# Kernel optimization log

Hardware: AMD Instinct MI355X
Metric: run time of the kernel (lower is better)

Reference implementation:

```python
import jax, jax.numpy as jnp
import numpy as np

B, S, IN_D, OUT_D, QD = 4, 1024, 16, 16, 32
HID, HEADS, HD, L, TED = 256, 8, 32, 4, 256
DECAY = 0.1
SCALE = HD ** -0.5


def _ln(x):
    m = x.mean(-1, keepdims=True)
    v = ((x - m) ** 2).mean(-1, keepdims=True)
    return (x - m) * jax.lax.rsqrt(v + 1e-5)


def _lin(x, w, b):
    # torch nn.Linear: y = x @ W^T + b, W is [out, in]
    return jnp.einsum('...i,oi->...o', x, w) + b


def _sin_emb(t, dim):
    half = dim // 2
    freqs = jnp.exp(-np.log(10000.0) * jnp.arange(half, dtype=jnp.float32) / (half - 1))
    a = t[:, None] * freqs[None, :]
    return jnp.concatenate([jnp.sin(a), jnp.cos(a)], axis=-1)


def _mish(x):
    return x * jnp.tanh(jax.nn.softplus(x))


def _gelu(x):
    return jax.nn.gelu(x, approximate=False)


def setup_inputs() -> dict:
    key = jax.random.key(0)
    ks = iter(jax.random.split(key, 64))

    def w(shape):
        return jax.random.normal(next(ks), shape, dtype=jnp.float32) * 0.02

    d = {}
    d['x'] = jax.random.normal(next(ks), (B, S, IN_D), dtype=jnp.float32)
    d['query'] = jax.random.normal(next(ks), (B, QD), dtype=jnp.float32)
    d['time'] = jax.random.uniform(next(ks), (B,), dtype=jnp.float32) * 1000.0
    d['tm_w1'] = w((TED * 4, TED)); d['tm_b1'] = jnp.zeros((TED * 4,), jnp.float32)
    d['tm_w2'] = w((TED, TED * 4)); d['tm_b2'] = jnp.zeros((TED,), jnp.float32)
    d['in_w'] = w((HID, IN_D)); d['in_b'] = jnp.zeros((HID,), jnp.float32)
    d['q_w1'] = w((HID, QD)); d['q_b1'] = jnp.zeros((HID,), jnp.float32)
    d['q_w2'] = w((HID, HID)); d['q_b2'] = jnp.zeros((HID,), jnp.float32)
    d['n1_w'] = jnp.ones((L, HID), jnp.float32); d['n1_b'] = jnp.zeros((L, HID), jnp.float32)
    d['qkv_w'] = w((L, 3 * HID, HID)); d['qkv_b'] = jnp.zeros((L, 3 * HID), jnp.float32)
    d['ap_w'] = w((L, HID, HID)); d['ap_b'] = jnp.zeros((L, HID), jnp.float32)
    d['rel_bias'] = w((L, 2 * S - 1, HEADS))
    d['n2_w'] = jnp.ones((L, HID), jnp.float32); d['n2_b'] = jnp.zeros((L, HID), jnp.float32)
    d['f1_w'] = w((L, 4 * HID, HID)); d['f1_b'] = jnp.zeros((L, 4 * HID), jnp.float32)
    d['f2_w'] = w((L, HID, 4 * HID)); d['f2_b'] = jnp.zeros((L, HID), jnp.float32)
    d['t1_w'] = w((L, HID, TED)); d['t1_b'] = jnp.zeros((L, HID), jnp.float32)
    d['t2_w'] = w((L, HID, HID)); d['t2_b'] = jnp.zeros((L, HID), jnp.float32)
    d['out_w'] = w((OUT_D, HID)); d['out_b'] = jnp.zeros((OUT_D,), jnp.float32)
    return d


def reference(x, query, time, tm_w1, tm_b1, tm_w2, tm_b2, in_w, in_b,
              q_w1, q_b1, q_w2, q_b2, n1_w, n1_b, qkv_w, qkv_b, ap_w, ap_b,
              rel_bias, n2_w, n2_b, f1_w, f1_b, f2_w, f2_b, t1_w, t1_b,
              t2_w, t2_b, out_w, out_b):
    Bx, Sx, _ = x.shape
    # time MLP: SinusoidalPosEmb -> Linear -> Mish -> Linear
    te = _lin(_sin_emb(time, TED), tm_w1, tm_b1)
    te = _lin(_mish(te), tm_w2, tm_b2)            # [B, TED]
    # input projection + query conditioning (relative-pos path: no abs pos emb)
    h = _lin(x, in_w, in_b)                        # [B, S, HID]
    qe = _lin(_gelu(_lin(query, q_w1, q_b1)), q_w2, q_b2)
    h = h + qe[:, None, :]
    # shared relative-distance structures
    idx = jnp.arange(Sx)
    rel = idx[:, None] - idx[None, :]              # [S, S]
    dec = jnp.exp(-DECAY * jnp.abs(rel).astype(jnp.float32))
    rel_idx = rel + S - 1                          # index into 2*max_seq_len-1 table
    for l in range(L):
        # time conditioning per block
        tp = _lin(_gelu(_lin(te, t1_w[l], t1_b[l])), t2_w[l], t2_b[l])
        xn = _ln(h + tp[:, None, :]) * n1_w[l] + n1_b[l]
        qkv = _lin(xn, qkv_w[l], qkv_b[l]).reshape(Bx, Sx, 3, HEADS, HD)
        qkv = qkv.transpose(2, 0, 3, 1, 4)          # [3, B, H, S, hd]
        q_, k_, v_ = qkv[0], qkv[1], qkv[2]
        attn = jnp.einsum('bhqd,bhkd->bhqk', q_, k_) * SCALE
        bias = rel_bias[l][rel_idx]                 # [S, S, H]
        attn = attn + (dec[:, :, None] * bias).transpose(2, 0, 1)[None]
        a = jax.nn.softmax(attn, axis=-1)
        o = jnp.einsum('bhqk,bhkd->bhqd', a, v_)
        o = o.transpose(0, 2, 1, 3).reshape(Bx, Sx, HID)
        h = h + _lin(o, ap_w[l], ap_b[l])           # residual from pre-time x
        xn2 = _ln(h) * n2_w[l] + n2_b[l]
        h = h + _lin(_gelu(_lin(xn2, f1_w[l], f1_b[l])), f2_w[l], f2_b[l])
    return _lin(h, out_w, out_b)
```

## Files before the change

kernel.cpp:

```cpp
#include <hip/hip_runtime.h>
#include <hip/hip_bf16.h>
#include <math.h>

#define S_LEN 1024
#define HID 256
#define HEADS 8
#define HD 32
#define NLAYER 4
#define TED 256
#define BATCH 4
#define DECAY 0.1f
#define ATT_SCALE 0.17677669529663687f
#define LOG2E 1.4426950408889634f

typedef __bf16 bf8_t __attribute__((ext_vector_type(8)));
typedef float f4_t __attribute__((ext_vector_type(4)));

__device__ __forceinline__ float gelu_f(float x) {
  return 0.5f * x * (1.f + erff(x * 0.70710678118654752f));
}
__device__ __forceinline__ __bf16 f2bf(float f) { return (__bf16)f; }

__global__ __launch_bounds__(256) void k_prep_a(
    const float* __restrict__ timev,
    const float* __restrict__ tm_w1, const float* __restrict__ tm_b1,
    const float* __restrict__ query,
    const float* __restrict__ q_w1, const float* __restrict__ q_b1,
    float* __restrict__ te1, float* __restrict__ q1) {
  int bid = blockIdx.x;
  int lane = threadIdx.x & 63;
  if (bid < 1024) {
    int r = bid * 4 + (threadIdx.x >> 6);
    int o = r & 1023, b = r >> 10;
    float t = timev[b];
    float ev[4];
#pragma unroll
    for (int e = 0; e < 4; e++) {
      int k = lane * 4 + e;
      int i = k & 127;
      float f = __expf(-logf(10000.f) * (float)i / 127.f);
      float a = t * f;
      ev[e] = (k < 128) ? sinf(a) : cosf(a);
    }
    const float* w = tm_w1 + (size_t)o * 256 + lane * 4;
    float4 w4 = *(const float4*)w;
    float s = ev[0] * w4.x + ev[1] * w4.y + ev[2] * w4.z + ev[3] * w4.w;
#pragma unroll
    for (int off = 32; off; off >>= 1) s += __shfl_xor(s, off);
    if (lane == 0) {
      s += tm_b1[o];
      float sp = (s > 20.f) ? s : log1pf(__expf(s));
      te1[r] = s * tanhf(sp);
    }
  } else {
    int r = (bid - 1024) * 4 + (threadIdx.x >> 6);
    int o = r & 255, b = r >> 8;
    float s = 0.f;
    if (lane < 8) {
      float4 a4 = *(const float4*)(query + b * 32 + lane * 4);
      float4 w4 = *(const float4*)(q_w1 + (size_t)o * 32 + lane * 4);
      s = a4.x * w4.x + a4.y * w4.y + a4.z * w4.z + a4.w * w4.w;
    }
#pragma unroll
    for (int off = 32; off; off >>= 1) s += __shfl_xor(s, off);
    if (lane == 0) q1[r] = gelu_f(s + q_b1[o]);
  }
}

__global__ __launch_bounds__(256) void k_prep_b(
    const float* __restrict__ te1, const float* __restrict__ tm_w2,
    const float* __restrict__ tm_b2,
    const float* __restrict__ q1, const float* __restrict__ q_w2,
    const float* __restrict__ q_b2,
    float* __restrict__ te, float* __restrict__ qe) {
  int bid = blockIdx.x;
  int lane = threadIdx.x & 63;
  bool iste = bid < 256;
  int r = (iste ? bid : bid - 256) * 4 + (threadIdx.x >> 6);
  int o = r & 255, b = r >> 8;
  int K = iste ? 1024 : 256;
  const float* a = (iste ? te1 : q1) + (size_t)b * K;
  const float* w = (iste ? tm_w2 : q_w2) + (size_t)o * K;
  float s = 0.f;
  for (int k = lane * 4; k < K; k += 256) {
    float4 a4 = *(const float4*)(a + k);
    float4 w4 = *(const float4*)(w + k);
    s += a4.x * w4.x + a4.y * w4.y + a4.z * w4.z + a4.w * w4.w;
  }
#pragma unroll
  for (int off = 32; off; off >>= 1) s += __shfl_xor(s, off);
  if (lane == 0) {
    s += (iste ? tm_b2 : q_b2)[o];
    (iste ? te : qe)[r] = s;
  }
}

template <int ACT, bool APG>
__global__ __launch_bounds__(256) void k_gemv(
    const float* __restrict__ A, const float* __restrict__ W,
    const float* __restrict__ bias, float* __restrict__ out,
    int K, int OUT) {
  int r = blockIdx.x * 4 + (threadIdx.x >> 6);
  int lane = threadIdx.x & 63;
  int o = r % OUT;
  int b = (r / OUT) % BATCH;
  int g = r / (OUT * BATCH);
  const float* a = A + (size_t)((APG ? g * BATCH : 0) + b) * K;
  const float* w = W + (size_t)(g * OUT + o) * K;
  float s = 0.f;
  for (int k = lane * 4; k < K; k += 256) {
    float4 a4 = *(const float4*)(a + k);
    float4 w4 = *(const float4*)(w + k);
    s += a4.x * w4.x + a4.y * w4.y + a4.z * w4.z + a4.w * w4.w;
  }
#pragma unroll
  for (int off = 32; off; off >>= 1) s += __shfl_xor(s, off);
  if (lane == 0) {
    s += bias[g * OUT + o];
    if (ACT == 1) s = gelu_f(s);
    if (ACT == 2) {
      float sp = (s > 20.f) ? s : log1pf(__expf(s));
      s = s * tanhf(sp);
    }
    out[r] = s;
  }
}

__global__ __launch_bounds__(256) void k_inproj(
    const float* __restrict__ x, const float* __restrict__ in_w,
    const float* __restrict__ in_b, const float* __restrict__ qe,
    float* __restrict__ h) {
  int row = blockIdx.x;
  int b = row >> 10;
  int j = threadIdx.x;
  __shared__ float xr[16];
  if (j < 16) xr[j] = x[row * 16 + j];
  __syncthreads();
  float s = in_b[j] + qe[b * 256 + j];
  const float* w = in_w + j * 16;
#pragma unroll
  for (int i = 0; i < 16; i++) s += xr[i] * w[i];
  h[(size_t)row * 256 + j] = s;
}

__global__ __launch_bounds__(256) void k_cvtall(
    const float* __restrict__ s0, __bf16* __restrict__ d0,
    const float* __restrict__ s1, __bf16* __restrict__ d1,
    const float* __restrict__ s2, __bf16* __restrict__ d2,
    const float* __restrict__ s3, __bf16* __restrict__ d3,
    const float* __restrict__ relb, float* __restrict__ decb_t) {
  int bid = blockIdx.x;
  if (bid >= 1536) {
    int lb = bid - 1536;
    int l = lb >> 6;
    int i = (lb & 63) * 256 + threadIdx.x;
    if (i < 2047 * 8) {
      int idx = i >> 3, hh = i & 7;
      float dec = __expf(-DECAY * fabsf((float)(idx - 1023)));
      decb_t[(l * 8 + hh) * 2048 + idx] = dec * relb[(size_t)l * 2047 * 8 + i] * LOG2E;
    }
    return;
  }
  const float* s; __bf16* d; int base;
  if (bid < 384)       { s = s0; d = d0; base = bid; }
  else if (bid < 512)  { s = s1; d = d1; base = bid - 384; }
  else if (bid < 1024) { s = s2; d = d2; base = bid - 512; }
  else                 { s = s3; d = d3; base = bid - 1024; }
  int i = (base * 256 + threadIdx.x) * 8;
  float4 a = *(const float4*)(s + i);
  float4 b = *(const float4*)(s + i + 4);
  bf8_t o;
  o[0] = f2bf(a.x); o[1] = f2bf(a.y); o[2] = f2bf(a.z); o[3] = f2bf(a.w);
  o[4] = f2bf(b.x); o[5] = f2bf(b.y); o[6] = f2bf(b.z); o[7] = f2bf(b.w);
  *(bf8_t*)(d + i) = o;
}

template <int BN, int ACT, int OUTMODE, bool HASTP>
__global__ __launch_bounds__(256) void k_gemm_lnf(
    const float* __restrict__ h, const __bf16* __restrict__ W,
    const float* __restrict__ bias, void* __restrict__ Cv,
    const float* __restrict__ tp, const float* __restrict__ lw,
    const float* __restrict__ lb, int N) {
  constexpr int K = 256;
  constexpr int NJ = (BN / 2) / 16;
  constexpr int BQ = BN / 64;
  __shared__ __bf16 Al[64 * 264];
  __shared__ __bf16 Bl[2 * BN * 32];
  int tid = threadIdx.x;
  int w = tid >> 6, lane = tid & 63;
  int g = lane >> 4, c = lane & 15;
  int n0 = blockIdx.x * BN, m0 = blockIdx.y * 64;

  int srow = tid >> 2;
  int scol = (tid & 3) * 8;
  int sw = (((tid & 3) ^ ((tid >> 3) & 3))) * 8;
  const __bf16* Wb = W + (size_t)n0 * K + scol;
  bf8_t nB[2][BQ];
#pragma unroll
  for (int sub = 0; sub < 2; sub++)
#pragma unroll
    for (int q = 0; q < BQ; q++)
      nB[sub][q] = *(const bf8_t*)(Wb + (size_t)(q * 64 + srow) * K + sub * 32);

  int sub32 = tid & 31, lrow = tid >> 5;
  int colb = sub32 * 8;
  float4 lw0 = *(const float4*)(lw + colb), lw1 = *(const float4*)(lw + colb + 4);
  float4 lb0 = *(const float4*)(lb + colb), lb1 = *(const float4*)(lb + colb + 4);
  float4 tp0, tp1;
  if (HASTP) {
    const float* tpr = tp + (m0 >> 10) * 256 + colb;
    tp0 = *(const float4*)tpr; tp1 = *(const float4*)(tpr + 4);
  }
#pragma unroll
  for (int p = 0; p < 8; p++) {
    int row = p * 8 + lrow;
    const float* hr = h + (size_t)(m0 + row) * 256 + colb;
    float4 a = *(const float4*)hr;
    float4 b2 = *(const float4*)(hr + 4);
    if (HASTP) {
      a.x += tp0.x; a.y += tp0.y; a.z += tp0.z; a.w += tp0.w;
      b2.x += tp1.x; b2.y += tp1.y; b2.z += tp1.z; b2.w += tp1.w;
    }
    float sum = a.x + a.y + a.z + a.w + b2.x + b2.y + b2.z + b2.w;
    float ss = a.x * a.x + a.y * a.y + a.z * a.z + a.w * a.w +
               b2.x * b2.x + b2.y * b2.y + b2.z * b2.z + b2.w * b2.w;
#pragma unroll
    for (int m = 1; m < 32; m <<= 1) {
      sum += __shfl_xor(sum, m);
      ss += __shfl_xor(ss, m);
    }
    float mean = sum * (1.f / 256.f);
    float var = ss * (1.f / 256.f) - mean * mean;
    float rs = rsqrtf(var + 1e-5f);
    bf8_t o;
    o[0] = f2bf((a.x - mean) * rs * lw0.x + lb0.x);
    o[1] = f2bf((a.y - mean) * rs * lw0.y + lb0.y);
    o[2] = f2bf((a.z - mean) * rs * lw0.z + lb0.z);
    o[3] = f2bf((a.w - mean) * rs * lw0.w + lb0.w);
    o[4] = f2bf((b2.x - mean) * rs * lw1.x + lb1.x);
    o[5] = f2bf((b2.y - mean) * rs * lw1.y + lb1.y);
    o[6] = f2bf((b2.z - mean) * rs * lw1.z + lb1.z);
    o[7] = f2bf((b2.w - mean) * rs * lw1.w + lb1.w);
    *(bf8_t*)&Al[row * 264 + colb] = o;
  }

  int wr = (w >> 1) * 32, wc = (w & 1) * (BN / 2);
  int aseg = ((g ^ ((c >> 1) & 3))) * 8;
  f4_t acc[2][NJ];
#pragma unroll
  for (int i = 0; i < 2; i++)
#pragma unroll
    for (int j = 0; j < NJ; j++) acc[i][j] = (f4_t){0.f, 0.f, 0.f, 0.f};

#pragma unroll
  for (int ph = 0; ph < 4; ph++) {
    __syncthreads();
#pragma unroll
    for (int sub = 0; sub < 2; sub++)
#pragma unroll
      for (int q = 0; q < BQ; q++)
        *(bf8_t*)&Bl[sub * BN * 32 + (q * 64 + srow) * 32 + sw] = nB[sub][q];
    __syncthreads();
    if (ph < 3) {
#pragma unroll
      for (int sub = 0; sub < 2; sub++)
#pragma unroll
        for (int q = 0; q < BQ; q++)
          nB[sub][q] = *(const bf8_t*)(Wb + (size_t)(q * 64 + srow) * K +
                                       (ph + 1) * 64 + sub * 32);
    }
#pragma unroll
    for (int sub = 0; sub < 2; sub++) {
      bf8_t af[2], bfr[NJ];
#pragma unroll
      for (int i = 0; i < 2; i++)
        af[i] = *(const bf8_t*)&Al[(wr + i * 16 + c) * 264 + ph * 64 + sub * 32 + g * 8];
#pragma unroll
      for (int j = 0; j < NJ; j++)
        bfr[j] = *(const bf8_t*)&Bl[sub * BN * 32 + (wc + j * 16 + c) * 32 + aseg];
#pragma unroll
      for (int i = 0; i < 2; i++)
#pragma unroll
        for (int j = 0; j < NJ; j++)
          acc[i][j] = __builtin_amdgcn_mfma_f32_16x16x32_bf16(af[i], bfr[j], acc[i][j], 0, 0, 0);
    }
  }
#pragma unroll
  for (int j = 0; j < NJ; j++) {
    int col = n0 + wc + j * 16 + c;
    float bv = bias[col];
#pragma unroll
    for (int i = 0; i < 2; i++) {
#pragma unroll
      for (int rr = 0; rr < 4; rr++) {
        int row = m0 + wr + i * 16 + 4 * g + rr;
        float v = acc[i][j][rr] + bv;
        if (ACT == 1) v = gelu_f(v);
        size_t idx = (size_t)row * N + col;
        if (OUTMODE == 1) ((float*)Cv)[idx] += v;
        else ((__bf16*)Cv)[idx] = f2bf(v);
      }
    }
  }
}

template <int BM, int BN, int ACT, int OUTMODE, int SPLITK, int KSTEPS>
__global__ __launch_bounds__(256) void k_gemm_mfma(
    const __bf16* __restrict__ A, const __bf16* __restrict__ W,
    const float* __restrict__ bias, void* __restrict__ Cv,
    int M, int N, int K) {
  constexpr int MI = (BM / 2) / 16, NJ = (BN / 2) / 16;
  constexpr int AQ = BM / 64, BQ = BN / 64;
  __shared__ __bf16 Al[BM * 32];
  __shared__ __bf16 Bl[BN * 32];
  int tid = threadIdx.x;
  int w = tid >> 6, lane = tid & 63;
  int g = lane >> 4, c = lane & 15;
  int n0 = blockIdx.x * BN, m0 = blockIdx.y * BM;
  int kbeg = blockIdx.z * KSTEPS * 32;
  int wr = (w >> 1) * (BM / 2), wc = (w & 1) * (BN / 2);
  int srow = tid >> 2;
  int scol = (tid & 3) * 8;
  int sw = (((tid & 3) ^ ((tid >> 3) & 3))) * 8;
  int aseg = ((g ^ ((c >> 1) & 3))) * 8;

  f4_t acc[MI][NJ];
#pragma unroll
  for (int i = 0; i < MI; i++)
#pragma unroll
    for (int j = 0; j < NJ; j++) acc[i][j] = (f4_t){0.f, 0.f, 0.f, 0.f};

  const __bf16* Ab = A + (size_t)m0 * K + scol + kbeg;
  const __bf16* Wb = W + (size_t)n0 * K + scol + kbeg;

  bf8_t nA[AQ], nB[BQ];
#pragma unroll
  for (int q = 0; q < AQ; q++)
    nA[q] = *(const bf8_t*)(Ab + (size_t)(q * 64 + srow) * K);
#pragma unroll
  for (int q = 0; q < BQ; q++)
    nB[q] = *(const bf8_t*)(Wb + (size_t)(q * 64 + srow) * K);

#pragma unroll
  for (int ks = 0; ks < KSTEPS; ks++) {
    __syncthreads();
#pragma unroll
    for (int q = 0; q < AQ; q++)
      *(bf8_t*)&Al[(q * 64 + srow) * 32 + sw] = nA[q];
#pragma unroll
    for (int q = 0; q < BQ; q++)
      *(bf8_t*)&Bl[(q * 64 + srow) * 32 + sw] = nB[q];
    __syncthreads();
    if (ks + 1 < KSTEPS) {
#pragma unroll
      for (int q = 0; q < AQ; q++)
        nA[q] = *(const bf8_t*)(Ab + (size_t)(q * 64 + srow) * K + (ks + 1) * 32);
#pragma unroll
      for (int q = 0; q < BQ; q++)
        nB[q] = *(const bf8_t*)(Wb + (size_t)(q * 64 + srow) * K + (ks + 1) * 32);
    }
    bf8_t af[MI], bfr[NJ];
#pragma unroll
    for (int i = 0; i < MI; i++)
      af[i] = *(const bf8_t*)&Al[(wr + i * 16 + c) * 32 + aseg];
#pragma unroll
    for (int j = 0; j < NJ; j++)
      bfr[j] = *(const bf8_t*)&Bl[(wc + j * 16 + c) * 32 + aseg];
#pragma unroll
    for (int i = 0; i < MI; i++)
#pragma unroll
      for (int j = 0; j < NJ; j++)
        acc[i][j] = __builtin_amdgcn_mfma_f32_16x16x32_bf16(af[i], bfr[j], acc[i][j], 0, 0, 0);
  }
#pragma unroll
  for (int j = 0; j < NJ; j++) {
    int col = n0 + wc + j * 16 + c;
    float bv = (SPLITK == 1 || blockIdx.z == 0) ? bias[col] : 0.f;
#pragma unroll
    for (int i = 0; i < MI; i++) {
#pragma unroll
      for (int r = 0; r < 4; r++) {
        int row = m0 + wr + i * 16 + 4 * g + r;
        float v = acc[i][j][r] + bv;
        if (ACT == 1) v = gelu_f(v);
        size_t idx = (size_t)row * N + col;
        if (OUTMODE == 1) {
          if (SPLITK == 1) ((float*)Cv)[idx] += v;
          else unsafeAtomicAdd(&((float*)Cv)[idx], v);
        } else if (OUTMODE == 0) ((float*)Cv)[idx] = v;
        else ((__bf16*)Cv)[idx] = f2bf(v);
      }
    }
  }
}

__global__ __launch_bounds__(256) void k_attn(
    const __bf16* __restrict__ qkv, const float* __restrict__ decb_t,
    __bf16* __restrict__ obuf) {
  __shared__ __bf16 Kl[64 * 40];
  __shared__ __bf16 Vt[32 * 72];
  __shared__ __bf16 Pl[4][16 * 72];
  __shared__ float db[1088];

  int tid = threadIdx.x;
  int w = tid >> 6, lane = tid & 63;
  int g = lane >> 4, c = lane & 15;
  int bh = blockIdx.y;
  int b = bh >> 3, hh = bh & 7;
  int q0 = blockIdx.x * 64;

  for (int i = tid; i < 1087; i += 256) db[i] = decb_t[hh * 2048 + q0 + i];

  bf8_t qraw = *(const bf8_t*)(qkv + ((size_t)(b * S_LEN + q0 + w * 16 + c)) * 768 + hh * 32 + 8 * g);
  bf8_t qfrag;
#pragma unroll
  for (int i = 0; i < 8; i++) qfrag[i] = f2bf((float)qraw[i] * (ATT_SCALE * LOG2E));

  float ps_acc[4] = {0.f, 0.f, 0.f, 0.f};
  f4_t o0 = {0.f, 0.f, 0.f, 0.f}, o1 = {0.f, 0.f, 0.f, 0.f};

  int rowb = w * 16 + 4 * g;
  __bf16* Plw = &Pl[w][0];

  int kvr = tid & 63, part = tid >> 6;
  const __bf16* base0 = qkv + ((size_t)(b * S_LEN + kvr)) * 768 + hh * 32 + part * 8;
  bf8_t k8 = *(const bf8_t*)(base0 + 256);
  bf8_t v8 = *(const bf8_t*)(base0 + 512);

  for (int c0 = 0; c0 < S_LEN; c0 += 64) {
    __syncthreads();
    {
      *(bf8_t*)&Kl[kvr * 40 + part * 8] = k8;
      int d0s = part * 8;
#pragma unroll
      for (int jj = 0; jj < 8; jj++) Vt[(d0s + jj) * 72 + kvr] = v8[jj];
    }
    __syncthreads();
    if (c0 + 64 < S_LEN) {
      const __bf16* basen = base0 + (size_t)(c0 + 64) * 768;
      k8 = *(const bf8_t*)(basen + 256);
      v8 = *(const bf8_t*)(basen + 512);
    }

    f4_t sc[4];
    f4_t zero4 = {0.f, 0.f, 0.f, 0.f};
#pragma unroll
    for (int j = 0; j < 4; j++) {
      bf8_t kfrag = *(const bf8_t*)&Kl[(j * 16 + c) * 40 + g * 8];
      sc[j] = __builtin_amdgcn_mfma_f32_16x16x32_bf16(qfrag, kfrag, zero4, 0, 0, 0);
    }
#pragma unroll
    for (int j = 0; j < 4; j++) {
      int bidx = rowb + 1023 - (c0 + j * 16 + c);
#pragma unroll
      for (int r = 0; r < 4; r++) {
        float p = exp2f(sc[j][r] + db[bidx + r]);
        ps_acc[r] += p;
        Plw[(4 * g + r) * 72 + j * 16 + c] = f2bf(p);
      }
    }
#pragma unroll
    for (int ss = 0; ss < 2; ss++) {
      bf8_t pa = *(const bf8_t*)&Plw[c * 72 + ss * 32 + g * 8];
      bf8_t v0 = *(const bf8_t*)&Vt[c * 72 + ss * 32 + g * 8];
      bf8_t v1 = *(const bf8_t*)&Vt[(c + 16) * 72 + ss * 32 + g * 8];
      o0 = __builtin_amdgcn_mfma_f32_16x16x32_bf16(pa, v0, o0, 0, 0, 0);
      o1 = __builtin_amdgcn_mfma_f32_16x16x32_bf16(pa, v1, o1, 0, 0, 0);
    }
  }

#pragma unroll
  for (int r = 0; r < 4; r++) {
#pragma unroll
    for (int m = 1; m < 16; m <<= 1) ps_acc[r] += __shfl_xor(ps_acc[r], m);
    float inv = 1.f / ps_acc[r];
    size_t rowg = (size_t)(b * S_LEN + q0 + rowb + r);
    obuf[rowg * 256 + hh * 32 + c] = f2bf(o0[r] * inv);
    obuf[rowg * 256 + hh * 32 + 16 + c] = f2bf(o1[r] * inv);
  }
}

__global__ __launch_bounds__(256) void k_out(
    const float* __restrict__ hbuf, const float* __restrict__ out_w,
    const float* __restrict__ out_b, float* __restrict__ out) {
  int tid = threadIdx.x;
  int r = blockIdx.x * 16 + (tid >> 4);
  int c = tid & 15;
  const float4* hr = (const float4*)(hbuf + (size_t)r * 256);
  const float4* w4 = (const float4*)(out_w + c * 256);
  float s = out_b[c];
#pragma unroll 8
  for (int k = 0; k < 64; k++) {
    float4 a = hr[k], b = w4[k];
    s += a.x * b.x + a.y * b.y + a.z * b.z + a.w * b.w;
  }
  out[r * 16 + c] = s;
}

extern "C" void kernel_launch(void* const* d_in, const int* in_sizes, int n_in,
                              void* d_out, int out_size, void* d_ws, size_t ws_size,
                              hipStream_t stream) {
  const float* x      = (const float*)d_in[0];
  const float* query  = (const float*)d_in[1];
  const float* timev  = (const float*)d_in[2];
  const float* tm_w1  = (const float*)d_in[3];
  const float* tm_b1  = (const float*)d_in[4];
  const float* tm_w2  = (const float*)d_in[5];
  const float* tm_b2  = (const float*)d_in[6];
  const float* in_w   = (const float*)d_in[7];
  const float* in_b   = (const float*)d_in[8];
  const float* q_w1   = (const float*)d_in[9];
  const float* q_b1   = (const float*)d_in[10];
  const float* q_w2   = (const float*)d_in[11];
  const float* q_b2   = (const float*)d_in[12];
  const float* n1_w   = (const float*)d_in[13];
  const float* n1_b   = (const float*)d_in[14];
  const float* qkv_w  = (const float*)d_in[15];
  const float* qkv_b  = (const float*)d_in[16];
  const float* ap_w   = (const float*)d_in[17];
  const float* ap_b   = (const float*)d_in[18];
  const float* relb   = (const float*)d_in[19];
  const float* n2_w   = (const float*)d_in[20];
  const float* n2_b   = (const float*)d_in[21];
  const float* f1_w   = (const float*)d_in[22];
  const float* f1_b   = (const float*)d_in[23];
  const float* f2_w   = (const float*)d_in[24];
  const float* f2_b   = (const float*)d_in[25];
  const float* t1_w   = (const float*)d_in[26];
  const float* t1_b   = (const float*)d_in[27];
  const float* t2_w   = (const float*)d_in[28];
  const float* t2_b   = (const float*)d_in[29];
  const float* out_w  = (const float*)d_in[30];
  const float* out_b  = (const float*)d_in[31];
  float* out = (float*)d_out;

  float* ws = (float*)d_ws;
  float*  h    = ws;
  __bf16* qkvb = (__bf16*)(ws + 1572864);
  __bf16* obb  = (__bf16*)(ws + 3145728);
  __bf16* y1b  = (__bf16*)(ws + 3670016);
  __bf16* wqkv = (__bf16*)(ws + 5767168);
  __bf16* wap  = (__bf16*)(ws + 6160384);
  __bf16* wf1  = (__bf16*)(ws + 6291456);
  __bf16* wf2  = (__bf16*)(ws + 6815744);
  float* decb  = ws + 7340032;
  float* qe    = decb + 65536;
  float* tp    = qe + 1024;
  float* te1   = tp + 4096;
  float* te    = te1 + 4096;
  float* q1    = te + 1024;
  float* tt    = q1 + 1024;

  k_cvtall<<<1792, 256, 0, stream>>>(qkv_w, wqkv, ap_w, wap, f1_w, wf1, f2_w, wf2,
                                     relb, decb);

  k_prep_a<<<1280, 256, 0, stream>>>(timev, tm_w1, tm_b1, query, q_w1, q_b1, te1, q1);
  k_prep_b<<<512, 256, 0, stream>>>(te1, tm_w2, tm_b2, q1, q_w2, q_b2, te, qe);
  k_gemv<1, false><<<1024, 256, 0, stream>>>(te, t1_w, t1_b, tt, 256, 256);
  k_gemv<0, true><<<1024, 256, 0, stream>>>(tt, t2_w, t2_b, tp, 256, 256);

  k_inproj<<<4096, 256, 0, stream>>>(x, in_w, in_b, qe, h);

  for (int l = 0; l < NLAYER; l++) {
    k_gemm_lnf<128, 0, 2, true><<<dim3(6, 64), 256, 0, stream>>>(
        h, wqkv + (size_t)l * 196608, qkv_b + l * 768, qkvb,
        tp + l * 1024, n1_w + l * 256, n1_b + l * 256, 768);
    k_attn<<<dim3(16, 32), 256, 0, stream>>>(qkvb, decb + l * 16384, obb);
    k_gemm_mfma<64, 64, 0, 1, 1, 8><<<dim3(4, 64), 256, 0, stream>>>(
        obb, wap + (size_t)l * 65536, ap_b + l * 256, h, 4096, 256, 256);
    k_gemm_lnf<128, 1, 2, false><<<dim3(8, 64), 256, 0, stream>>>(
        h, wf1 + (size_t)l * 262144, f1_b + l * 1024, y1b,
        nullptr, n2_w + l * 256, n2_b + l * 256, 1024);
    k_gemm_mfma<64, 64, 0, 1, 4, 8><<<dim3(4, 64, 4), 256, 0, stream>>>(
        y1b, wf2 + (size_t)l * 262144, f2_b + l * 256, h, 4096, 256, 1024);
  }
  k_out<<<256, 256, 0, stream>>>(h, out_w, out_b, out);
}
```

Measured before the change: 329.6 us.

## Fuse attention projection, LayerNorm, and MLP into one per-row-tile kernel

Replaces the three per-layer launches (attention output projection, LN plus FC1 with GELU, and split-K FC2) with one kernel. Each 512-thread block owns 16 rows and keeps the normalized activations and the 1024-wide GELU intermediate in shared memory, streaming weights through a double-register prefetch. This removes the y1 global round trip, the split-K atomics and two launches. The cost is that only 256 blocks run, each re-reading the full weight matrices, and the large LDS footprint may limit occupancy.

```diff
diff --git a/kernel.cpp b/kernel.cpp
--- a/kernel.cpp
+++ b/kernel.cpp
@@ -304,96 +304,6 @@
   }
 }
 
-template <int BM, int BN, int ACT, int OUTMODE, int SPLITK, int KSTEPS>
-__global__ __launch_bounds__(256) void k_gemm_mfma(
-    const __bf16* __restrict__ A, const __bf16* __restrict__ W,
-    const float* __restrict__ bias, void* __restrict__ Cv,
-    int M, int N, int K) {
-  constexpr int MI = (BM / 2) / 16, NJ = (BN / 2) / 16;
-  constexpr int AQ = BM / 64, BQ = BN / 64;
-  __shared__ __bf16 Al[BM * 32];
-  __shared__ __bf16 Bl[BN * 32];
-  int tid = threadIdx.x;
-  int w = tid >> 6, lane = tid & 63;
-  int g = lane >> 4, c = lane & 15;
-  int n0 = blockIdx.x * BN, m0 = blockIdx.y * BM;
-  int kbeg = blockIdx.z * KSTEPS * 32;
-  int wr = (w >> 1) * (BM / 2), wc = (w & 1) * (BN / 2);
-  int srow = tid >> 2;
-  int scol = (tid & 3) * 8;
-  int sw = (((tid & 3) ^ ((tid >> 3) & 3))) * 8;
-  int aseg = ((g ^ ((c >> 1) & 3))) * 8;
-
-  f4_t acc[MI][NJ];
-#pragma unroll
-  for (int i = 0; i < MI; i++)
-#pragma unroll
-    for (int j = 0; j < NJ; j++) acc[i][j] = (f4_t){0.f, 0.f, 0.f, 0.f};
-
-  const __bf16* Ab = A + (size_t)m0 * K + scol + kbeg;
-  const __bf16* Wb = W + (size_t)n0 * K + scol + kbeg;
-
-  bf8_t nA[AQ], nB[BQ];
-#pragma unroll
-  for (int q = 0; q < AQ; q++)
-    nA[q] = *(const bf8_t*)(Ab + (size_t)(q * 64 + srow) * K);
-#pragma unroll
-  for (int q = 0; q < BQ; q++)
-    nB[q] = *(const bf8_t*)(Wb + (size_t)(q * 64 + srow) * K);
-
-#pragma unroll
-  for (int ks = 0; ks < KSTEPS; ks++) {
-    __syncthreads();
-#pragma unroll
-    for (int q = 0; q < AQ; q++)
-      *(bf8_t*)&Al[(q * 64 + srow) * 32 + sw] = nA[q];
-#pragma unroll
-    for (int q = 0; q < BQ; q++)
-      *(bf8_t*)&Bl[(q * 64 + srow) * 32 + sw] = nB[q];
-    __syncthreads();
-    if (ks + 1 < KSTEPS) {
-#pragma unroll
-      for (int q = 0; q < AQ; q++)
-        nA[q] = *(const bf8_t*)(Ab + (size_t)(q * 64 + srow) * K + (ks + 1) * 32);
-#pragma unroll
-      for (int q = 0; q < BQ; q++)
-        nB[q] = *(const bf8_t*)(Wb + (size_t)(q * 64 + srow) * K + (ks + 1) * 32);
-    }
-    bf8_t af[MI], bfr[NJ];
-#pragma unroll
-    for (int i = 0; i < MI; i++)
-      af[i] = *(const bf8_t*)&Al[(wr + i * 16 + c) * 32 + aseg];
-#pragma unroll
-    for (int j = 0; j < NJ; j++)
-      bfr[j] = *(const bf8_t*)&Bl[(wc + j * 16 + c) * 32 + aseg];
-#pragma unroll
-    for (int i = 0; i < MI; i++)
-#pragma unroll
-      for (int j = 0; j < NJ; j++)
-        acc[i][j] = __builtin_amdgcn_mfma_f32_16x16x32_bf16(af[i], bfr[j], acc[i][j], 0, 0, 0);
-  }
-#pragma unroll
-  for (int j = 0; j < NJ; j++) {
-    int col = n0 + wc + j * 16 + c;
-    float bv = (SPLITK == 1 || blockIdx.z == 0) ? bias[col] : 0.f;
-#pragma unroll
-    for (int i = 0; i < MI; i++) {
-#pragma unroll
-      for (int r = 0; r < 4; r++) {
-        int row = m0 + wr + i * 16 + 4 * g + r;
-        float v = acc[i][j][r] + bv;
-        if (ACT == 1) v = gelu_f(v);
-        size_t idx = (size_t)row * N + col;
-        if (OUTMODE == 1) {
-          if (SPLITK == 1) ((float*)Cv)[idx] += v;
-          else unsafeAtomicAdd(&((float*)Cv)[idx], v);
-        } else if (OUTMODE == 0) ((float*)Cv)[idx] = v;
-        else ((__bf16*)Cv)[idx] = f2bf(v);
-      }
-    }
-  }
-}
-
 __global__ __launch_bounds__(256) void k_attn(
     const __bf16* __restrict__ qkv, const float* __restrict__ decb_t,
     __bf16* __restrict__ obuf) {
@@ -477,6 +387,161 @@
     size_t rowg = (size_t)(b * S_LEN + q0 + rowb + r);
     obuf[rowg * 256 + hh * 32 + c] = f2bf(o0[r] * inv);
     obuf[rowg * 256 + hh * 32 + 16 + c] = f2bf(o1[r] * inv);
+  }
+}
+
+__global__ __launch_bounds__(512) void k_back(
+    const __bf16* __restrict__ obb, float* __restrict__ h,
+    const __bf16* __restrict__ wap, const float* __restrict__ apb,
+    const float* __restrict__ n2w, const float* __restrict__ n2b,
+    const __bf16* __restrict__ wf1, const float* __restrict__ f1b,
+    const __bf16* __restrict__ wf2, const float* __restrict__ f2b) {
+  __shared__ __bf16 Asm[16 * 264];
+  __shared__ __bf16 Bl[2 * 256 * 32];
+  __shared__ __bf16 y1l[16 * 1032];
+  __shared__ float red[16][8][2];
+
+  int tid = threadIdx.x;
+  int w = tid >> 6, lane = tid & 63;
+  int g = lane >> 4, c = lane & 15;
+  int m0 = blockIdx.x * 16;
+  int srow = tid >> 2;
+  int scol = (tid & 3) * 8;
+  int sw = (((tid & 3) ^ ((srow >> 1) & 3))) * 8;
+  int wc = w * 32;
+  int axor = (c >> 1) & 3;
+  int boff0 = (wc + c) * 32 + ((g ^ axor)) * 8;
+  int boff1 = (wc + 16 + c) * 32 + ((g ^ axor)) * 8;
+  int col0 = wc + c, col1 = wc + 16 + c;
+  f4_t zero4 = {0.f, 0.f, 0.f, 0.f};
+
+  bf8_t nB[2][2];
+  auto prefetch = [&](const __bf16* base, int K, int ko) {
+#pragma unroll
+    for (int s = 0; s < 2; s++)
+#pragma unroll
+      for (int q = 0; q < 2; q++)
+        nB[s][q] = *(const bf8_t*)(base + (size_t)(q * 128 + srow) * K + ko + s * 32 + scol);
+  };
+  auto stageB = [&]() {
+    __syncthreads();
+#pragma unroll
+    for (int s = 0; s < 2; s++)
+#pragma unroll
+      for (int q = 0; q < 2; q++)
+        *(bf8_t*)&Bl[s * 8192 + (q * 128 + srow) * 32 + sw] = nB[s][q];
+    __syncthreads();
+  };
+  f4_t a0, a1;
+  auto mstep = [&](const __bf16* Ab, int AS, int ko) {
+#pragma unroll
+    for (int s = 0; s < 2; s++) {
+      bf8_t af = *(const bf8_t*)&Ab[c * AS + ko + s * 32 + g * 8];
+      bf8_t b0 = *(const bf8_t*)&Bl[s * 8192 + boff0];
+      bf8_t b1 = *(const bf8_t*)&Bl[s * 8192 + boff1];
+      a0 = __builtin_amdgcn_mfma_f32_16x16x32_bf16(af, b0, a0, 0, 0, 0);
+      a1 = __builtin_amdgcn_mfma_f32_16x16x32_bf16(af, b1, a1, 0, 0, 0);
+    }
+  };
+
+  prefetch(wap, 256, 0);
+  {
+    int row = tid >> 5, gr = tid & 31;
+    *(bf8_t*)&Asm[row * 264 + gr * 8] = *(const bf8_t*)(obb + (size_t)(m0 + row) * 256 + gr * 8);
+  }
+
+  a0 = zero4; a1 = zero4;
+#pragma unroll
+  for (int ph = 0; ph < 4; ph++) {
+    stageB();
+    if (ph < 3) prefetch(wap, 256, (ph + 1) * 64);
+    else prefetch(wf1, 256, 0);
+    mstep(Asm, 264, ph * 64);
+  }
+
+  float hn[2][4];
+  {
+    float b0v = apb[col0], b1v = apb[col1];
+    float ps[4], pq[4];
+#pragma unroll
+    for (int r = 0; r < 4; r++) {
+      size_t row = (size_t)(m0 + 4 * g + r);
+      float v0 = a0[r] + b0v + h[row * 256 + col0];
+      float v1 = a1[r] + b1v + h[row * 256 + col1];
+      h[row * 256 + col0] = v0;
+      h[row * 256 + col1] = v1;
+      hn[0][r] = v0; hn[1][r] = v1;
+      ps[r] = v0 + v1;
+      pq[r] = v0 * v0 + v1 * v1;
+    }
+#pragma unroll
+    for (int r = 0; r < 4; r++) {
+#pragma unroll
+      for (int m = 1; m < 16; m <<= 1) {
+        ps[r] += __shfl_xor(ps[r], m);
+        pq[r] += __shfl_xor(pq[r], m);
+      }
+    }
+    if (c == 0) {
+#pragma unroll
+      for (int r = 0; r < 4; r++) {
+        red[4 * g + r][w][0] = ps[r];
+        red[4 * g + r][w][1] = pq[r];
+      }
+    }
+  }
+  __syncthreads();
+  {
+    float n2w0 = n2w[col0], n2b0 = n2b[col0];
+    float n2w1 = n2w[col1], n2b1 = n2b[col1];
+#pragma unroll
+    for (int r = 0; r < 4; r++) {
+      int row = 4 * g + r;
+      float S = 0.f, Q = 0.f;
+#pragma unroll
+      for (int ww = 0; ww < 8; ww++) { S += red[row][ww][0]; Q += red[row][ww][1]; }
+      float mean = S * (1.f / 256.f);
+      float var = Q * (1.f / 256.f) - mean * mean;
+      float rs = rsqrtf(var + 1e-5f);
+      Asm[row * 264 + col0] = f2bf((hn[0][r] - mean) * rs * n2w0 + n2b0);
+      Asm[row * 264 + col1] = f2bf((hn[1][r] - mean) * rs * n2w1 + n2b1);
+    }
+  }
+
+#pragma unroll
+  for (int nc = 0; nc < 4; nc++) {
+    a0 = zero4; a1 = zero4;
+#pragma unroll
+    for (int ph = 0; ph < 4; ph++) {
+      stageB();
+      if (ph < 3) prefetch(wf1 + nc * 65536, 256, (ph + 1) * 64);
+      else if (nc < 3) prefetch(wf1 + (nc + 1) * 65536, 256, 0);
+      else prefetch(wf2, 1024, 0);
+      mstep(Asm, 264, ph * 64);
+    }
+    float b0v = f1b[nc * 256 + col0], b1v = f1b[nc * 256 + col1];
+#pragma unroll
+    for (int r = 0; r < 4; r++) {
+      y1l[(4 * g + r) * 1032 + nc * 256 + col0] = f2bf(gelu_f(a0[r] + b0v));
+      y1l[(4 * g + r) * 1032 + nc * 256 + col1] = f2bf(gelu_f(a1[r] + b1v));
+    }
+  }
+
+  a0 = zero4; a1 = zero4;
+#pragma unroll
+  for (int ph = 0; ph < 16; ph++) {
+    stageB();
+    if (ph < 15) prefetch(wf2, 1024, (ph + 1) * 64);
+    mstep(y1l, 1032, ph * 64);
+  }
+  {
+    float b0v = f2b[col0], b1v = f2b[col1];
+#pragma unroll
+    for (int r = 0; r < 4; r++) {
+      size_t row = (size_t)(m0 + 4 * g + r);
+      h[row * 256 + col0] += a0[r] + b0v;
+      h[row * 256 + col1] += a1[r] + b1v;
+    }
   }
 }
 
@@ -538,7 +603,6 @@
   float*  h    = ws;
   __bf16* qkvb = (__bf16*)(ws + 1572864);
   __bf16* obb  = (__bf16*)(ws + 3145728);
-  __bf16* y1b  = (__bf16*)(ws + 3670016);
   __bf16* wqkv = (__bf16*)(ws + 5767168);
   __bf16* wap  = (__bf16*)(ws + 6160384);
   __bf16* wf1  = (__bf16*)(ws + 6291456);
@@ -566,13 +630,11 @@
         h, wqkv + (size_t)l * 196608, qkv_b + l * 768, qkvb,
         tp + l * 1024, n1_w + l * 256, n1_b + l * 256, 768);
     k_attn<<<dim3(16, 32), 256, 0, stream>>>(qkvb, decb + l * 16384, obb);
-    k_gemm_mfma<64, 64, 0, 1, 1, 8><<<dim3(4, 64), 256, 0, stream>>>(
-        obb, wap + (size_t)l * 65536, ap_b + l * 256, h, 4096, 256, 256);
-    k_gemm_lnf<128, 1, 2, false><<<dim3(8, 64), 256, 0, stream>>>(
-        h, wf1 + (size_t)l * 262144, f1_b + l * 1024, y1b,
-        nullptr, n2_w + l * 256, n2_b + l * 256, 1024);
-    k_gemm_mfma<64, 64, 0, 1, 4, 8><<<dim3(4, 64, 4), 256, 0, stream>>>(
-        y1b, wf2 + (size_t)l * 262144, f2_b + l * 256, h, 4096, 256, 1024);
+    k_back<<<256, 512, 0, stream>>>(
+        obb, h, wap + (size_t)l * 65536, ap_b + l * 256,
+        n2_w + l * 256, n2_b + l * 256,
+        wf1 + (size_t)l * 262144, f1_b + l * 1024,
+        wf2 + (size_t)l * 262144, f2_b + l * 256);
   }
   k_out<<<256, 256, 0, stream>>>(h, out_w, out_b, out);
 }
```

Result: faster. 282.7 us (-14.2%).
